# Kernel optimization log

Measured on AMD Instinct MI355X. Metric: run time of the kernel, lower is better.

## Reference

```python
import jax, jax.numpy as jnp
import numpy as np

D = 768        # memory_dim
H = 16         # num_heads
DH = D // H    # head dim (hidden_size)
SCALING = 0.25 # inverse temperature beta
STEPS = 5      # update_steps_max (fixed-count; eps early-exit ignored)
TOP_K = 4
LN_EPS = 1e-5


def setup_inputs() -> dict:
    key = jax.random.key(0)
    ks = jax.random.split(key, 8)
    B, N = 2, 100000
    inp = {
        "query_embedding": jax.random.normal(ks[0], (B, D), jnp.float32),
        "memory": jax.random.normal(ks[1], (N, D), jnp.float32),
        # LayerNorm (affine) params: state pattern (query), stored pattern (keys), pattern projection (values)
        "ln_q_g": jnp.ones((D,), jnp.float32), "ln_q_b": jnp.zeros((D,), jnp.float32),
        "ln_s_g": jnp.ones((D,), jnp.float32), "ln_s_b": jnp.zeros((D,), jnp.float32),
        "ln_p_g": jnp.ones((D,), jnp.float32), "ln_p_b": jnp.zeros((D,), jnp.float32),
        # association-space projections and output projection
        "Wq": 0.02 * jax.random.normal(ks[2], (D, D), jnp.float32), "bq": jnp.zeros((D,), jnp.float32),
        "Wk": 0.02 * jax.random.normal(ks[3], (D, D), jnp.float32), "bk": jnp.zeros((D,), jnp.float32),
        "Wv": 0.02 * jax.random.normal(ks[4], (D, D), jnp.float32), "bv": jnp.zeros((D,), jnp.float32),
        "Wo": 0.02 * jax.random.normal(ks[5], (D, D), jnp.float32), "bo": jnp.zeros((D,), jnp.float32),
    }
    return inp


def _layer_norm(x, g, b):
    m = jnp.mean(x, axis=-1, keepdims=True)
    v = jnp.var(x, axis=-1, keepdims=True)
    return (x - m) * jax.lax.rsqrt(v + LN_EPS) * g + b


def _hopfield_pool(query, memory, ln_q_g, ln_q_b, ln_s_g, ln_s_b, ln_p_g, ln_p_b,
                   Wq, bq, Wk, bk, Wv, bv, Wo, bo):
    B = query.shape[0]
    # projections (memory is shared across the batch, so project once: (N, D))
    q0 = _layer_norm(query, ln_q_g, ln_q_b) @ Wq + bq        # (B, D)
    k = (_layer_norm(memory, ln_s_g, ln_s_b) @ Wk + bk).reshape(-1, H, DH)   # (N, H, DH)
    v = (_layer_norm(memory, ln_p_g, ln_p_b) @ Wv + bv).reshape(-1, H, DH)   # (N, H, DH)

    q = (SCALING * q0).reshape(B, H, DH)                      # (B, H, DH)
    attn = jax.nn.softmax(jnp.einsum("bhd,nhd->bhn", q, k), axis=-1)
    for _ in range(STEPS):  # iterative Hopfield state updates
        q = SCALING * jnp.einsum("bhn,nhd->bhd", attn, k)
        attn = jax.nn.softmax(jnp.einsum("bhd,nhd->bhn", q, k), axis=-1)
    out = jnp.einsum("bhn,nhd->bhd", attn, v).reshape(B, D)   # concat heads
    return out @ Wo + bo                                      # (B, D) pooled


def reference(query_embedding, memory, ln_q_g, ln_q_b, ln_s_g, ln_s_b, ln_p_g, ln_p_b,
              Wq, bq, Wk, bk, Wv, bv, Wo, bo):
    pooled = _hopfield_pool(query_embedding, memory, ln_q_g, ln_q_b, ln_s_g, ln_s_b,
                            ln_p_g, ln_p_b, Wq, bq, Wk, bk, Wv, bv, Wo, bo)
    pooled_norm = pooled / jnp.linalg.norm(pooled, axis=-1, keepdims=True)
    memory_norm = memory / jnp.linalg.norm(memory, axis=-1, keepdims=True)
    similarities = pooled_norm @ memory_norm.T                # (B, N)
    _, top_indices = jax.lax.top_k(similarities, TOP_K)       # (B, TOP_K)
    return top_indices, pooled
```

## Files before the change

kernel.cpp:

```cpp
#include <hip/hip_runtime.h>
#include <cstdio>
#include <cstdint>


#define NMEM 100000
#define NPAD 100096
#define HOPB 1024
#define CBLK 98
#define UKS  512
#define UROWS 196
#define SCALING_ 0.25f

typedef __attribute__((ext_vector_type(8))) short bf16x8;
typedef __attribute__((ext_vector_type(4))) float f32x4;

__device__ __forceinline__ unsigned short f2bf(float f) {
  union { float f; unsigned u; } c; c.f = f;
  unsigned u = c.u + 0x7fffu + ((c.u >> 16) & 1u);
  return (unsigned short)(u >> 16);
}
__device__ __forceinline__ float bf2f(unsigned short h) {
  union { unsigned u; float f; } c; c.u = ((unsigned)h) << 16;
  return c.f;
}
__device__ __forceinline__ void gl_lds16(const void* g, void* l) {
  __builtin_amdgcn_global_load_lds(
      (const __attribute__((address_space(1))) unsigned int*)g,
      (__attribute__((address_space(3))) unsigned int*)l, 16, 0, 0);
}

__device__ __forceinline__ bool bet(float s, int n, float v, int i) {
  return (s > v) || (s == v && n < i);
}
struct Top4 {
  float v0, v1, v2, v3;
  int   i0, i1, i2, i3;
  __device__ __forceinline__ void init() {
    v0 = v1 = v2 = v3 = -INFINITY;
    i0 = i1 = i2 = i3 = 0x7fffffff;
  }
  __device__ __forceinline__ void ins(float s, int n) {
    bool c0 = bet(s, n, v0, i0), c1 = bet(s, n, v1, i1);
    bool c2 = bet(s, n, v2, i2), c3 = bet(s, n, v3, i3);
    float w0 = c0 ? s : v0;             int j0 = c0 ? n : i0;
    float w1 = c0 ? v0 : (c1 ? s : v1); int j1 = c0 ? i0 : (c1 ? n : i1);
    float w2 = c1 ? v1 : (c2 ? s : v2); int j2 = c1 ? i1 : (c2 ? n : i2);
    float w3 = c2 ? v2 : (c3 ? s : v3); int j3 = c2 ? i2 : (c3 ? n : i3);
    v0 = w0; v1 = w1; v2 = w2; v3 = w3;
    i0 = j0; i1 = j1; i2 = j2; i3 = j3;
  }
};
__device__ __forceinline__ void bfly(Top4& a, int omax) {
  for (int o = omax; o >= 1; o >>= 1) {
    float w0 = __shfl_xor(a.v0, o), w1 = __shfl_xor(a.v1, o);
    float w2 = __shfl_xor(a.v2, o), w3 = __shfl_xor(a.v3, o);
    int   j0 = __shfl_xor(a.i0, o), j1 = __shfl_xor(a.i1, o);
    int   j2 = __shfl_xor(a.i2, o), j3 = __shfl_xor(a.i3, o);
    a.ins(w0, j0); a.ins(w1, j1); a.ins(w2, j2); a.ins(w3, j3);
  }
}

__global__ __launch_bounds__(256) void k_fold_wt(const float* __restrict__ Wk,
                                                 const float* __restrict__ Wv,
                                                 const float* __restrict__ gs,
                                                 const float* __restrict__ gp,
                                                 unsigned short* __restrict__ WT) {
  __shared__ float ts[64][65];
  int d0 = blockIdx.x * 64, j0 = blockIdx.y * 64, z = blockIdx.z;
  const float* W = z ? Wv : Wk;
  const float* g = z ? gp : gs;
  int t = threadIdx.x, c = t & 63, r4 = t >> 6;
#pragma unroll
  for (int p = 0; p < 16; ++p) {
    int r = p * 4 + r4;
    ts[r][c] = g[d0 + r] * W[(size_t)(d0 + r) * 768 + j0 + c];
  }
  __syncthreads();
#pragma unroll
  for (int p = 0; p < 16; ++p) {
    int jr = p * 4 + r4;
    WT[(size_t)(z * 768 + j0 + jr) * 768 + d0 + c] = f2bf(ts[c][jr]);
  }
}

__global__ __launch_bounds__(256) void k_fold_bias(const float* __restrict__ Wk,
                                                   const float* __restrict__ Wv,
                                                   const float* __restrict__ bs,
                                                   const float* __restrict__ bp,
                                                   float* __restrict__ PB) {
  int jc = blockIdx.x, dz = blockIdx.y, t = threadIdx.x;
  int j = jc * 256 + t;
  const float* W  = (j < 768) ? Wk : Wv;
  const float* bb = (j < 768) ? bs : bp;
  int jj = (j < 768) ? j : j - 768;
  float a = 0.f;
  int dend = dz * 96 + 96;
  for (int d = dz * 96; d < dend; ++d) a = fmaf(bb[d], W[(size_t)d * 768 + jj], a);
  PB[dz * 1536 + j] = a;
}

__global__ __launch_bounds__(256) void k_bias_red(const float* __restrict__ PB,
                                                  const float* __restrict__ bk,
                                                  const float* __restrict__ bv,
                                                  float* __restrict__ BKV) {
  int j = blockIdx.x * 256 + threadIdx.x;
  float a = (j < 768) ? bk[j] : bv[j - 768];
#pragma unroll
  for (int dz = 0; dz < 8; ++dz) a += PB[dz * 1536 + j];
  BKV[j] = a;
}

__global__ __launch_bounds__(256) void k_q0(const float* __restrict__ qe,
                                            const float* __restrict__ gq,
                                            const float* __restrict__ bq_ln,
                                            const float* __restrict__ Wq,
                                            const float* __restrict__ bq,
                                            float* __restrict__ qbuf) {
  int b = blockIdx.y, jc = blockIdx.x, t = threadIdx.x;
  __shared__ float xs[768];
  __shared__ float sred[16];
  __shared__ float pr[256];
  float x0 = qe[b * 768 + t], x1 = qe[b * 768 + 256 + t], x2 = qe[b * 768 + 512 + t];
  float s = x0 + x1 + x2, s2 = x0 * x0 + x1 * x1 + x2 * x2;
#pragma unroll
  for (int o = 32; o >= 1; o >>= 1) { s += __shfl_xor(s, o); s2 += __shfl_xor(s2, o); }
  int lane = t & 63, w = t >> 6;
  if (lane == 0) { sred[w] = s; sred[8 + w] = s2; }
  __syncthreads();
  s  = sred[0] + sred[1] + sred[2] + sred[3];
  s2 = sred[8] + sred[9] + sred[10] + sred[11];
  float mean = s * (1.f / 768.f);
  float var  = s2 * (1.f / 768.f) - mean * mean;
  float rstd = rsqrtf(var + 1e-5f);
  xs[t]       = (x0 - mean) * rstd * gq[t]       + bq_ln[t];
  xs[t + 256] = (x1 - mean) * rstd * gq[t + 256] + bq_ln[t + 256];
  xs[t + 512] = (x2 - mean) * rstd * gq[t + 512] + bq_ln[t + 512];
  __syncthreads();
  int j = jc * 64 + lane;
  float a = 0.f;
  int d0 = w * 192;
  for (int d = d0; d < d0 + 192; ++d) a = fmaf(xs[d], Wq[(size_t)d * 768 + j], a);
  pr[t] = a;
  __syncthreads();
  if (t < 64) {
    float sv = pr[t] + pr[64 + t] + pr[128 + t] + pr[192 + t];
    int j2 = jc * 64 + t;
    qbuf[b * 768 + j2] = SCALING_ * (sv + bq[j2]);
  }
}

__global__ __launch_bounds__(256) void k_ln(const float* __restrict__ mem,
                                            unsigned short* __restrict__ XH,
                                            float* __restrict__ rnorm) {
  int gw = (blockIdx.x * 256 + threadIdx.x) >> 6;
  int lane = threadIdx.x & 63;
  int n0 = gw * 25;
  int nend = n0 + 25; if (nend > NPAD) nend = NPAD;
  for (int n = n0; n < nend; ++n) {
    ushort4* orow = (ushort4*)(XH + (size_t)n * 768);
    if (n >= NMEM) {
      ushort4 z; z.x = z.y = z.z = z.w = 0;
      orow[lane] = z; orow[lane + 64] = z; orow[lane + 128] = z;
      continue;
    }
    const float4* r = (const float4*)(mem + (size_t)n * 768);
    float4 x0 = r[lane], x1 = r[lane + 64], x2 = r[lane + 128];
    float s  = x0.x + x0.y + x0.z + x0.w + x1.x + x1.y + x1.z + x1.w +
               x2.x + x2.y + x2.z + x2.w;
    float s2 = x0.x * x0.x + x0.y * x0.y + x0.z * x0.z + x0.w * x0.w +
               x1.x * x1.x + x1.y * x1.y + x1.z * x1.z + x1.w * x1.w +
               x2.x * x2.x + x2.y * x2.y + x2.z * x2.z + x2.w * x2.w;
#pragma unroll
    for (int o = 32; o >= 1; o >>= 1) { s += __shfl_xor(s, o); s2 += __shfl_xor(s2, o); }
    float mean = s * (1.f / 768.f);
    float var  = s2 * (1.f / 768.f) - mean * mean;
    float rstd = rsqrtf(var + 1e-5f);
    if (lane == 0) rnorm[n] = rsqrtf(s2);
    ushort4 o0, o1, o2;
    o0.x = f2bf((x0.x - mean) * rstd); o0.y = f2bf((x0.y - mean) * rstd);
    o0.z = f2bf((x0.z - mean) * rstd); o0.w = f2bf((x0.w - mean) * rstd);
    o1.x = f2bf((x1.x - mean) * rstd); o1.y = f2bf((x1.y - mean) * rstd);
    o1.z = f2bf((x1.z - mean) * rstd); o1.w = f2bf((x1.w - mean) * rstd);
    o2.x = f2bf((x2.x - mean) * rstd); o2.y = f2bf((x2.y - mean) * rstd);
    o2.z = f2bf((x2.z - mean) * rstd); o2.w = f2bf((x2.w - mean) * rstd);
    orow[lane] = o0; orow[lane + 64] = o1; orow[lane + 128] = o2;
  }
}

__global__ __launch_bounds__(256) void k_gemm(const unsigned short* __restrict__ XH,
                                              const unsigned short* __restrict__ WT,
                                              const float* __restrict__ BKV,
                                              unsigned short* __restrict__ KB) {
  __shared__ __align__(16) unsigned short SM[32768];
  int f = blockIdx.x;
  int xcd = f & 7, s = f >> 3;
  int g = s / 6, jt = s - g * 6;
  int mt = g * 8 + xcd;
  if (mt >= 782) return;
  int m0 = mt * 128, j0 = jt * 128;
  int tid = threadIdx.x;
  int wave = tid >> 6, lane = tid & 63;
  int wm = wave >> 1, wn = wave & 1;
  int fr_r = lane & 15, chb = lane >> 4;
  f32x4 acc[4][4] = {};

  auto stage = [&](int kt, int bb) {
    unsigned short* As = SM + bb * 16384;
    unsigned short* Bs = As + 8192;
    int k0 = kt * 64;
#pragma unroll
    for (int it = 0; it < 4; ++it) {
      int c = it * 256 + tid;
      int row = c >> 3, kk = c & 7;
      int src = (kk ^ (row & 7)) * 8;
      gl_lds16(XH + (size_t)(m0 + row) * 768 + k0 + src, As + c * 8);
      gl_lds16(WT + (size_t)(j0 + row) * 768 + k0 + src, Bs + c * 8);
    }
  };

  stage(0, 0);
  int cur = 0;
  for (int kt = 0; kt < 12; ++kt) {
    if (kt < 11) {
      stage(kt + 1, cur ^ 1);
      asm volatile("s_waitcnt vmcnt(8)" ::: "memory");
    } else {
      asm volatile("s_waitcnt vmcnt(0)" ::: "memory");
    }
    __builtin_amdgcn_s_barrier();
    __builtin_amdgcn_sched_barrier(0);
    const unsigned short* As = SM + cur * 16384;
    const unsigned short* Bs = As + 8192;
    __builtin_amdgcn_s_setprio(1);
#pragma unroll
    for (int ks = 0; ks < 2; ++ks) {
      bf16x8 af[4], bfr[4];
#pragma unroll
      for (int ff = 0; ff < 4; ++ff) {
        int ra = wm * 64 + ff * 16 + fr_r;
        int rb = wn * 64 + ff * 16 + fr_r;
        int cha  = ((ks * 4 + chb) ^ (ra & 7)) * 8;
        int chbb = ((ks * 4 + chb) ^ (rb & 7)) * 8;
        af[ff]  = *(const bf16x8*)(As + ra * 64 + cha);
        bfr[ff] = *(const bf16x8*)(Bs + rb * 64 + chbb);
      }
#pragma unroll
      for (int fm = 0; fm < 4; ++fm)
#pragma unroll
        for (int fn = 0; fn < 4; ++fn)
          acc[fm][fn] = __builtin_amdgcn_mfma_f32_16x16x32_bf16(af[fm], bfr[fn],
                                                                acc[fm][fn], 0, 0, 0);
    }
    __builtin_amdgcn_s_setprio(0);
    __builtin_amdgcn_s_barrier();
    __builtin_amdgcn_sched_barrier(0);
    cur ^= 1;
  }
  int cr = (lane >> 4) * 4, cc = lane & 15;
#pragma unroll
  for (int fm = 0; fm < 4; ++fm)
#pragma unroll
    for (int fn = 0; fn < 4; ++fn) {
      int col = wn * 64 + fn * 16 + cc;
      float bias = BKV[j0 + col];
      int rb = (wm * 64 + fm * 16 + cr) * 128 + col;
#pragma unroll
      for (int i = 0; i < 4; ++i)
        SM[rb + i * 128] = f2bf(acc[fm][fn][i] + bias);
    }
  __syncthreads();
#pragma unroll
  for (int it = 0; it < 8; ++it) {
    int c = it * 256 + tid;
    int row = c >> 4, cg = c & 15;
    *(bf16x8*)(KB + (size_t)(m0 + row) * 768 + j0 + cg * 8) =
        *(const bf16x8*)(SM + row * 128 + cg * 8);
  }
}

__device__ __forceinline__ void load6(const unsigned short* p, float* o) {
  ushort2 a = *(const ushort2*)(p);
  ushort2 b = *(const ushort2*)(p + 2);
  ushort2 c = *(const ushort2*)(p + 4);
  o[0] = bf2f(a.x); o[1] = bf2f(a.y);
  o[2] = bf2f(b.x); o[3] = bf2f(b.y);
  o[4] = bf2f(c.x); o[5] = bf2f(c.y);
}

__global__ __launch_bounds__(256) void k_hop(const unsigned short* __restrict__ KB,
                                             const float* __restrict__ qin,
                                             float* __restrict__ pa,
                                             float* __restrict__ pl) {
  __shared__ float red[4][768];
  __shared__ float redl[4][128];
  int tid = threadIdx.x, blk = blockIdx.x;
  int w = tid >> 6, lane = tid & 63;
  int hb = w & 1, sub = w >> 1;
  float qv0[6], qv1[6];
  const float* qb = qin + hb * 384 + lane * 6;
#pragma unroll
  for (int j = 0; j < 6; ++j) { qv0[j] = qb[j]; qv1[j] = qb[768 + j]; }
  float l0 = 0.f, l1 = 0.f;
  float acc0[6] = {}, acc1[6] = {};
  int n0 = blk * CBLK + sub * 49;
  int nend = n0 + 49;
  if (nend > NMEM) nend = NMEM;
#pragma unroll 4
  for (int n = n0; n < nend; ++n) {
    const unsigned short* ks = KB + (size_t)n * 768 + hb * 384 + lane * 6;
    float kf[6]; load6(ks, kf);
    float sc0 = 0.f, sc1 = 0.f;
#pragma unroll
    for (int j = 0; j < 6; ++j) {
      sc0 = fmaf(kf[j], qv0[j], sc0);
      sc1 = fmaf(kf[j], qv1[j], sc1);
    }
#pragma unroll
    for (int o = 1; o < 8; o <<= 1) {
      sc0 += __shfl_xor(sc0, o);
      sc1 += __shfl_xor(sc1, o);
    }
    float e0 = __expf(sc0);
    float e1 = __expf(sc1);
    l0 += e0; l1 += e1;
#pragma unroll
    for (int j = 0; j < 6; ++j) {
      acc0[j] = fmaf(e0, kf[j], acc0[j]);
      acc1[j] = fmaf(e1, kf[j], acc1[j]);
    }
  }
#pragma unroll
  for (int j = 0; j < 6; ++j) {
    red[w][lane * 12 + j]     = acc0[j];
    red[w][lane * 12 + 6 + j] = acc1[j];
  }
  redl[w][lane * 2]     = l0;
  redl[w][lane * 2 + 1] = l1;
  __syncthreads();
  if (sub == 0) {
#pragma unroll
    for (int j = 0; j < 6; ++j) {
      acc0[j] += red[w + 2][lane * 12 + j];
      acc1[j] += red[w + 2][lane * 12 + 6 + j];
    }
    l0 += redl[w + 2][lane * 2];
    l1 += redl[w + 2][lane * 2 + 1];
    int h = hb * 8 + (lane >> 3), p = lane & 7;
    size_t b0 = ((size_t)(h * 2 + 0) * HOPB + blk) * 48 + p * 6;
    size_t b1 = ((size_t)(h * 2 + 1) * HOPB + blk) * 48 + p * 6;
#pragma unroll
    for (int j = 0; j < 6; ++j) { pa[b0 + j] = acc0[j]; pa[b1 + j] = acc1[j]; }
    if (p == 0) {
      pl[(size_t)(h * 2 + 0) * HOPB + blk] = l0;
      pl[(size_t)(h * 2 + 1) * HOPB + blk] = l1;
    }
  }
}

__global__ __launch_bounds__(256) void k_hred(const float* __restrict__ pa,
                                              const float* __restrict__ pl,
                                              float* __restrict__ qout) {
  int b = blockIdx.x & 1, h = blockIdx.x >> 1;
  __shared__ float sred[4];
  __shared__ float p3[256];
  int t = threadIdx.x, lane = t & 63, w = t >> 6;
  size_t mlb = (size_t)(h * 2 + b) * HOPB;
  float ll = 0.f;
  for (int i = t; i < HOPB; i += 256) ll += pl[mlb + i];
#pragma unroll
  for (int o = 32; o >= 1; o >>= 1) ll += __shfl_xor(ll, o);
  if (lane == 0) sred[w] = ll;
  __syncthreads();
  float ltot = sred[0] + sred[1] + sred[2] + sred[3];
  int d = t & 63, seg = t >> 6;
  float a = 0.f;
  if (d < 48) {
#pragma unroll 4
    for (int i = seg; i < HOPB; i += 4)
      a += pa[(mlb + i) * 48 + d];
  }
  p3[seg * 64 + d] = a;
  __syncthreads();
  if (t < 48) {
    float av = p3[t] + p3[64 + t] + p3[128 + t] + p3[192 + t];
    qout[b * 768 + h * 48 + t] = SCALING_ * (av / ltot);
  }
}

__global__ __launch_bounds__(256) void k_escore(const unsigned short* __restrict__ KB,
                                                const float* __restrict__ qin,
                                                float* __restrict__ S,
                                                float* __restrict__ pl) {
  __shared__ float redl[4][128];
  int tid = threadIdx.x, blk = blockIdx.x;
  int w = tid >> 6, lane = tid & 63;
  int hb = w & 1, sub = w >> 1;
  float qv0[6], qv1[6];
  const float* qb = qin + hb * 384 + lane * 6;
#pragma unroll
  for (int j = 0; j < 6; ++j) { qv0[j] = qb[j]; qv1[j] = qb[768 + j]; }
  float l0 = 0.f, l1 = 0.f;
  int hl = lane >> 3, p = lane & 7;
  int h = hb * 8 + hl;
  int n0 = blk * CBLK + sub * 49;
  int nend = n0 + 49;
  if (nend > NMEM) nend = NMEM;
#pragma unroll 4
  for (int n = n0; n < nend; ++n) {
    const unsigned short* ks = KB + (size_t)n * 768 + hb * 384 + lane * 6;
    float kf[6]; load6(ks, kf);
    float sc0 = 0.f, sc1 = 0.f;
#pragma unroll
    for (int j = 0; j < 6; ++j) {
      sc0 = fmaf(kf[j], qv0[j], sc0);
      sc1 = fmaf(kf[j], qv1[j], sc1);
    }
#pragma unroll
    for (int o = 1; o < 8; o <<= 1) {
      sc0 += __shfl_xor(sc0, o);
      sc1 += __shfl_xor(sc1, o);
    }
    if (p == 0) {
      S[(size_t)n * 32 + h]      = sc0;
      S[(size_t)n * 32 + 16 + h] = sc1;
    }
    l0 += __expf(sc0);
    l1 += __expf(sc1);
  }
  redl[w][lane * 2]     = l0;
  redl[w][lane * 2 + 1] = l1;
  __syncthreads();
  if (sub == 0) {
    l0 += redl[w + 2][lane * 2];
    l1 += redl[w + 2][lane * 2 + 1];
    if (p == 0) {
      pl[(size_t)(h * 2 + 0) * HOPB + blk] = l0;
      pl[(size_t)(h * 2 + 1) * HOPB + blk] = l1;
    }
  }
}

__global__ __launch_bounds__(256) void k_hredM(const float* __restrict__ pl,
                                               float* __restrict__ C) {
  int b = blockIdx.x & 1, h = blockIdx.x >> 1;
  __shared__ float sred[4];
  int t = threadIdx.x, lane = t & 63, w = t >> 6;
  size_t mlb = (size_t)(h * 2 + b) * HOPB;
  float ll = 0.f;
  for (int i = t; i < HOPB; i += 256) ll += pl[mlb + i];
#pragma unroll
  for (int o = 32; o >= 1; o >>= 1) ll += __shfl_xor(ll, o);
  if (lane == 0) sred[w] = ll;
  __syncthreads();
  if (t == 0) C[b * 16 + h] = logf(sred[0] + sred[1] + sred[2] + sred[3]);
}

__global__ __launch_bounds__(256) void k_upass(const unsigned short* __restrict__ XH,
                                               const float* __restrict__ S,
                                               const float* __restrict__ C,
                                               float* __restrict__ UP) {
  __shared__ float SW[64 * 32];
  __shared__ float cc[32];
  int kb = blockIdx.x, t = threadIdx.x;
  if (t < 32) cc[t] = C[t];
  float a0[32], a1[32], a2[32];
#pragma unroll
  for (int i = 0; i < 32; ++i) { a0[i] = 0.f; a1[i] = 0.f; a2[i] = 0.f; }
  int n0 = kb * UROWS;
  int nend = n0 + UROWS; if (nend > NMEM) nend = NMEM;
  for (int ns = n0; ns < nend; ns += 64) {
    int sub = nend - ns; if (sub > 64) sub = 64;
    __syncthreads();
    for (int i = t; i < sub * 32; i += 256)
      SW[i] = __expf(S[(size_t)ns * 32 + i] - cc[i & 31]);
    __syncthreads();
    for (int r = 0; r < sub; ++r) {
      const unsigned short* xr = XH + (size_t)(ns + r) * 768;
      float x0 = bf2f(xr[t]), x1 = bf2f(xr[t + 256]), x2 = bf2f(xr[t + 512]);
      const float4* w4 = (const float4*)(SW + r * 32);
#pragma unroll
      for (int c = 0; c < 8; ++c) {
        float4 wv = w4[c];
        a0[c * 4 + 0] = fmaf(wv.x, x0, a0[c * 4 + 0]);
        a0[c * 4 + 1] = fmaf(wv.y, x0, a0[c * 4 + 1]);
        a0[c * 4 + 2] = fmaf(wv.z, x0, a0[c * 4 + 2]);
        a0[c * 4 + 3] = fmaf(wv.w, x0, a0[c * 4 + 3]);
        a1[c * 4 + 0] = fmaf(wv.x, x1, a1[c * 4 + 0]);
        a1[c * 4 + 1] = fmaf(wv.y, x1, a1[c * 4 + 1]);
        a1[c * 4 + 2] = fmaf(wv.z, x1, a1[c * 4 + 2]);
        a1[c * 4 + 3] = fmaf(wv.w, x1, a1[c * 4 + 3]);
        a2[c * 4 + 0] = fmaf(wv.x, x2, a2[c * 4 + 0]);
        a2[c * 4 + 1] = fmaf(wv.y, x2, a2[c * 4 + 1]);
        a2[c * 4 + 2] = fmaf(wv.z, x2, a2[c * 4 + 2]);
        a2[c * 4 + 3] = fmaf(wv.w, x2, a2[c * 4 + 3]);
      }
    }
  }
#pragma unroll
  for (int bh = 0; bh < 32; ++bh) {
    size_t base = ((size_t)kb * 32 + bh) * 768;
    UP[base + t]       = a0[bh];
    UP[base + 256 + t] = a1[bh];
    UP[base + 512 + t] = a2[bh];
  }
}

__global__ __launch_bounds__(256) void k_ured(const float* __restrict__ UP,
                                              float* __restrict__ U) {
  int o = blockIdx.x * 256 + threadIdx.x;
  float s0 = 0.f, s1 = 0.f, s2 = 0.f, s3 = 0.f;
#pragma unroll 4
  for (int kb = 0; kb < UKS; kb += 4) {
    s0 += UP[(size_t)(kb + 0) * 24576 + o];
    s1 += UP[(size_t)(kb + 1) * 24576 + o];
    s2 += UP[(size_t)(kb + 2) * 24576 + o];
    s3 += UP[(size_t)(kb + 3) * 24576 + o];
  }
  U[o] = (s0 + s1) + (s2 + s3);
}

__global__ __launch_bounds__(256) void k_outproj(const float* __restrict__ U,
                                                 const unsigned short* __restrict__ WT,
                                                 const float* __restrict__ BKV,
                                                 float* __restrict__ outa) {
  int gw = blockIdx.x * 4 + (threadIdx.x >> 6);
  int lane = threadIdx.x & 63;
  int b = gw >= 768;
  int j = gw - b * 768;
  int h = j / 48;
  const float* u = U + (size_t)(b * 16 + h) * 768;
  const unsigned short* wr = WT + (size_t)(768 + j) * 768;
  float a = 0.f;
  for (int d = lane; d < 768; d += 64) a = fmaf(u[d], bf2f(wr[d]), a);
#pragma unroll
  for (int o = 32; o >= 1; o >>= 1) a += __shfl_xor(a, o);
  if (lane == 0) outa[b * 768 + j] = a + BKV[768 + j];
}

__global__ __launch_bounds__(256) void k_pooled(const float* __restrict__ outa,
                                                const float* __restrict__ Wo,
                                                const float* __restrict__ bo,
                                                float* __restrict__ dp) {
  __shared__ float xs[768];
  __shared__ float pr[256];
  int b = blockIdx.y, jc = blockIdx.x, t = threadIdx.x;
  xs[t]       = outa[b * 768 + t];
  xs[t + 256] = outa[b * 768 + 256 + t];
  xs[t + 512] = outa[b * 768 + 512 + t];
  __syncthreads();
  int w = t >> 6, lane = t & 63;
  int j = jc * 64 + lane;
  float a = 0.f;
  int d0 = w * 192;
  for (int d = d0; d < d0 + 192; ++d) a = fmaf(xs[d], Wo[(size_t)d * 768 + j], a);
  pr[t] = a;
  __syncthreads();
  if (t < 64) {
    float sv = pr[t] + pr[64 + t] + pr[128 + t] + pr[192 + t];
    int j2 = jc * 64 + t;
    dp[b * 768 + j2] = sv + bo[j2];
  }
}

__global__ __launch_bounds__(256) void k_pnorm(const float* __restrict__ dp,
                                               float* __restrict__ PN) {
  int b = blockIdx.x, t = threadIdx.x;
  __shared__ float sred[8];
  float x0 = dp[b * 768 + t], x1 = dp[b * 768 + 256 + t], x2 = dp[b * 768 + 512 + t];
  float s2 = x0 * x0 + x1 * x1 + x2 * x2;
#pragma unroll
  for (int o = 32; o >= 1; o >>= 1) s2 += __shfl_xor(s2, o);
  int lane = t & 63, w = t >> 6;
  if (lane == 0) sred[w] = s2;
  __syncthreads();
  float tot = sred[0] + sred[1] + sred[2] + sred[3];
  float rs = rsqrtf(tot);
  PN[b * 768 + t]       = x0 * rs;
  PN[b * 768 + 256 + t] = x1 * rs;
  PN[b * 768 + 512 + t] = x2 * rs;
}

__global__ __launch_bounds__(256) void k_sim(const float* __restrict__ mem,
                                             const float* __restrict__ PN,
                                             const float* __restrict__ rnorm,
                                             float* __restrict__ tval,
                                             int* __restrict__ tidx) {
  int gw = (blockIdx.x * 256 + threadIdx.x) >> 6;
  int lane = threadIdx.x & 63;
  const float4* pa = (const float4*)(PN);
  const float4* pb = (const float4*)(PN + 768);
  float4 qa0 = pa[lane], qa1 = pa[lane + 64], qa2 = pa[lane + 128];
  float4 qb0 = pb[lane], qb1 = pb[lane + 64], qb2 = pb[lane + 128];
  Top4 t0, t1; t0.init(); t1.init();
  int n0 = gw * 13;
  int nend = n0 + 13; if (nend > NMEM) nend = NMEM;
  for (int n = n0; n < nend; ++n) {
    const float4* r = (const float4*)(mem + (size_t)n * 768);
    float4 x0 = r[lane], x1 = r[lane + 64], x2 = r[lane + 128];
    float d0 = x0.x * qa0.x + x0.y * qa0.y + x0.z * qa0.z + x0.w * qa0.w +
               x1.x * qa1.x + x1.y * qa1.y + x1.z * qa1.z + x1.w * qa1.w +
               x2.x * qa2.x + x2.y * qa2.y + x2.z * qa2.z + x2.w * qa2.w;
    float d1 = x0.x * qb0.x + x0.y * qb0.y + x0.z * qb0.z + x0.w * qb0.w +
               x1.x * qb1.x + x1.y * qb1.y + x1.z * qb1.z + x1.w * qb1.w +
               x2.x * qb2.x + x2.y * qb2.y + x2.z * qb2.z + x2.w * qb2.w;
#pragma unroll
    for (int o = 32; o >= 1; o >>= 1) { d0 += __shfl_xor(d0, o); d1 += __shfl_xor(d1, o); }
    float rn = rnorm[n];
    t0.ins(d0 * rn, n);
    t1.ins(d1 * rn, n);
  }
  if (lane == 0) {
    int base = gw * 8;
    tval[base + 0] = t0.v0; tval[base + 1] = t0.v1; tval[base + 2] = t0.v2; tval[base + 3] = t0.v3;
    tval[base + 4] = t1.v0; tval[base + 5] = t1.v1; tval[base + 6] = t1.v2; tval[base + 7] = t1.v3;
    tidx[base + 0] = t0.i0; tidx[base + 1] = t0.i1; tidx[base + 2] = t0.i2; tidx[base + 3] = t0.i3;
    tidx[base + 4] = t1.i0; tidx[base + 5] = t1.i1; tidx[base + 6] = t1.i2; tidx[base + 7] = t1.i3;
  }
}

__global__ __launch_bounds__(256) void k_top1(const float* __restrict__ tval,
                                              const int* __restrict__ tidx,
                                              float* __restrict__ ptv,
                                              int* __restrict__ pti) {
  __shared__ float lv[4][8];
  __shared__ int   li[4][8];
  int z = blockIdx.x, t = threadIdx.x;
  int lane = t & 63, w = t >> 6;
  int wv = z * 256 + t;
  Top4 a, b; a.init(); b.init();
#pragma unroll
  for (int r = 0; r < 4; ++r) {
    a.ins(tval[wv * 8 + r],     tidx[wv * 8 + r]);
    b.ins(tval[wv * 8 + 4 + r], tidx[wv * 8 + 4 + r]);
  }
  bfly(a, 32);
  bfly(b, 32);
  if (lane == 0) {
    lv[w][0] = a.v0; lv[w][1] = a.v1; lv[w][2] = a.v2; lv[w][3] = a.v3;
    lv[w][4] = b.v0; lv[w][5] = b.v1; lv[w][6] = b.v2; lv[w][7] = b.v3;
    li[w][0] = a.i0; li[w][1] = a.i1; li[w][2] = a.i2; li[w][3] = a.i3;
    li[w][4] = b.i0; li[w][5] = b.i1; li[w][6] = b.i2; li[w][7] = b.i3;
  }
  __syncthreads();
  if (t < 2) {
    Top4 m_; m_.init();
#pragma unroll
    for (int w2 = 0; w2 < 4; ++w2)
#pragma unroll
      for (int r = 0; r < 4; ++r) m_.ins(lv[w2][t * 4 + r], li[w2][t * 4 + r]);
    int base = z * 8 + t * 4;
    ptv[base + 0] = m_.v0; ptv[base + 1] = m_.v1;
    ptv[base + 2] = m_.v2; ptv[base + 3] = m_.v3;
    pti[base + 0] = m_.i0; pti[base + 1] = m_.i1;
    pti[base + 2] = m_.i2; pti[base + 3] = m_.i3;
  }
}

__global__ __launch_bounds__(64) void k_top2(const float* __restrict__ ptv,
                                             const int* __restrict__ pti,
                                             float* __restrict__ dout) {
  int t = threadIdx.x;
  int half = t >> 5, e = t & 31;
  Top4 a; a.init();
#pragma unroll
  for (int r = 0; r < 4; ++r)
    a.ins(ptv[e * 8 + half * 4 + r], pti[e * 8 + half * 4 + r]);
  bfly(a, 16);
  if (e == 0) {
    dout[half * 4 + 0] = (float)a.i0;
    dout[half * 4 + 1] = (float)a.i1;
    dout[half * 4 + 2] = (float)a.i2;
    dout[half * 4 + 3] = (float)a.i3;
  }
}

extern "C" void kernel_launch(void* const* d_in, const int* in_sizes, int n_in,
                              void* d_out, int out_size, void* d_ws, size_t ws_size,
                              hipStream_t stream) {
  const float* qe     = (const float*)d_in[0];
  const float* mem    = (const float*)d_in[1];
  const float* ln_q_g = (const float*)d_in[2];
  const float* ln_q_b = (const float*)d_in[3];
  const float* ln_s_g = (const float*)d_in[4];
  const float* ln_s_b = (const float*)d_in[5];
  const float* ln_p_g = (const float*)d_in[6];
  const float* ln_p_b = (const float*)d_in[7];
  const float* Wq = (const float*)d_in[8];  const float* bq = (const float*)d_in[9];
  const float* Wk = (const float*)d_in[10]; const float* bk = (const float*)d_in[11];
  const float* Wv = (const float*)d_in[12]; const float* bv = (const float*)d_in[13];
  const float* Wo = (const float*)d_in[14]; const float* bo = (const float*)d_in[15];

  char* w = (char*)d_ws;
  size_t off = 0;
  auto alloc = [&](size_t bytes) {
    size_t o = off;
    off += (bytes + 255) & ~(size_t)255;
    return o;
  };
  unsigned short* WT   = (unsigned short*)(w + alloc((size_t)1536 * 768 * 2));
  float*          PB   = (float*)(w + alloc(8 * 1536 * 4));
  float*          BKV  = (float*)(w + alloc(1536 * 4));
  float*          QBUF = (float*)(w + alloc(1536 * 4));
  float*          OUTA = (float*)(w + alloc(1536 * 4));
  float*          PN   = (float*)(w + alloc(1536 * 4));
  float*          CML  = (float*)(w + alloc(32 * 4));
  float*          UBUF = (float*)(w + alloc((size_t)24576 * 4));
  float*          RNORM= (float*)(w + alloc((size_t)NPAD * 4));
  unsigned short* XH   = (unsigned short*)(w + alloc((size_t)NPAD * 768 * 2));
  unsigned short* KB   = (unsigned short*)(w + alloc((size_t)NPAD * 768 * 2));
  float*          PA   = (float*)(w + alloc((size_t)32 * HOPB * 48 * 4));
  float*          PL   = (float*)(w + alloc((size_t)32 * HOPB * 4));
  float*          SB   = (float*)(w + alloc((size_t)NMEM * 32 * 4));
  float*          UP   = (float*)(w + alloc((size_t)UKS * 24576 * 4));
  float*          TVAL = (float*)(w + alloc((size_t)8192 * 8 * 4));
  int*            TIDX = (int*)(w + alloc((size_t)8192 * 8 * 4));
  float*          PTV  = (float*)(w + alloc((size_t)32 * 8 * 4));
  int*            PTI  = (int*)(w + alloc((size_t)32 * 8 * 4));
  if (off > ws_size) {
    fprintf(stderr, "[hopfield] ws too small: need %zu have %zu\n", off, ws_size);
    return;
  }
  float* dout = (float*)d_out;

  k_fold_wt  <<<dim3(12, 12, 2), 256, 0, stream>>>(Wk, Wv, ln_s_g, ln_p_g, WT);
  k_fold_bias<<<dim3(6, 8), 256, 0, stream>>>(Wk, Wv, ln_s_b, ln_p_b, PB);
  k_bias_red <<<6, 256, 0, stream>>>(PB, bk, bv, BKV);
  k_q0       <<<dim3(12, 2), 256, 0, stream>>>(qe, ln_q_g, ln_q_b, Wq, bq, QBUF);
  k_ln       <<<1024, 256, 0, stream>>>(mem, XH, RNORM);
  k_gemm     <<<98 * 6 * 8, 256, 0, stream>>>(XH, WT, BKV, KB);
  for (int step = 0; step < 5; ++step) {
    k_hop    <<<HOPB, 256, 0, stream>>>(KB, QBUF, PA, PL);
    k_hred   <<<32, 256, 0, stream>>>(PA, PL, QBUF);
  }
  k_escore   <<<HOPB, 256, 0, stream>>>(KB, QBUF, SB, PL);
  k_hredM    <<<32, 256, 0, stream>>>(PL, CML);
  k_upass    <<<UKS, 256, 0, stream>>>(XH, SB, CML, UP);
  k_ured     <<<96, 256, 0, stream>>>(UP, UBUF);
  k_outproj  <<<384, 256, 0, stream>>>(UBUF, WT, BKV, OUTA);
  k_pooled   <<<dim3(12, 2), 256, 0, stream>>>(OUTA, Wo, bo, dout + 8);
  k_pnorm    <<<2, 256, 0, stream>>>(dout + 8, PN);
  k_sim      <<<2048, 256, 0, stream>>>(mem, PN, RNORM, TVAL, TIDX);
  k_top1     <<<32, 256, 0, stream>>>(TVAL, TIDX, PTV, PTI);
  k_top2     <<<1, 64, 0, stream>>>(PTV, PTI, dout);
}
```

Measured before the change: 851.1 us.

## Replace per-step reduction kernels with atomic accumulation into rotating buffers

Removes the separate k_hred and k_hredM reduction kernels. Each k_hop and k_escore block now atomically adds its partial accumulators and softmax denominators into small per-step buffers. The next step folds the normalization (scaling/L) into its query load, and block 0 zeroes the buffer two steps ahead. This cuts six kernel launches and the large partial-sum round trips through memory, at the cost of global atomic contention and a nondeterministic summation order.

```diff
diff --git a/kernel.cpp b/kernel.cpp
--- a/kernel.cpp
+++ b/kernel.cpp
@@ -115,11 +115,16 @@
                                             const float* __restrict__ bq_ln,
                                             const float* __restrict__ Wq,
                                             const float* __restrict__ bq,
-                                            float* __restrict__ qbuf) {
+                                            float* __restrict__ ACCb,
+                                            float* __restrict__ Lb) {
   int b = blockIdx.y, jc = blockIdx.x, t = threadIdx.x;
   __shared__ float xs[768];
   __shared__ float sred[16];
   __shared__ float pr[256];
+  if (jc == 0 && b == 0) {
+    for (int i = t; i < 1536; i += 256) ACCb[1536 + i] = 0.f;
+    if (t < 32) { Lb[t] = 1.0f; Lb[32 + t] = 0.f; }
+  }
   float x0 = qe[b * 768 + t], x1 = qe[b * 768 + 256 + t], x2 = qe[b * 768 + 512 + t];
   float s = x0 + x1 + x2, s2 = x0 * x0 + x1 * x1 + x2 * x2;
 #pragma unroll
@@ -145,7 +150,8 @@
   if (t < 64) {
     float sv = pr[t] + pr[64 + t] + pr[128 + t] + pr[192 + t];
     int j2 = jc * 64 + t;
-    qbuf[b * 768 + j2] = SCALING_ * (sv + bq[j2]);
+    int h = j2 / 48, dh = j2 - h * 48;
+    ACCb[(h * 2 + b) * 48 + dh] = sv + bq[j2];
   }
 }
 
@@ -288,18 +294,31 @@
 }
 
 __global__ __launch_bounds__(256) void k_hop(const unsigned short* __restrict__ KB,
-                                             const float* __restrict__ qin,
-                                             float* __restrict__ pa,
-                                             float* __restrict__ pl) {
+                                             float* __restrict__ ACCb,
+                                             float* __restrict__ Lb,
+                                             int s) {
   __shared__ float red[4][768];
   __shared__ float redl[4][128];
   int tid = threadIdx.x, blk = blockIdx.x;
   int w = tid >> 6, lane = tid & 63;
   int hb = w & 1, sub = w >> 1;
+  const float* Ap  = ACCb + s * 1536;
+  const float* Lp  = Lb + s * 32;
+  float* An  = ACCb + (s + 1) * 1536;
+  float* Ln_ = Lb + (s + 1) * 32;
+  if (blk == 0) {
+    for (int i = tid; i < 1536; i += 256) ACCb[(s + 2) * 1536 + i] = 0.f;
+    if (tid < 32) Lb[(s + 2) * 32 + tid] = 0.f;
+  }
+  int h = hb * 8 + (lane >> 3), p = lane & 7;
+  float rl0 = SCALING_ / Lp[h * 2 + 0];
+  float rl1 = SCALING_ / Lp[h * 2 + 1];
   float qv0[6], qv1[6];
-  const float* qb = qin + hb * 384 + lane * 6;
-#pragma unroll
-  for (int j = 0; j < 6; ++j) { qv0[j] = qb[j]; qv1[j] = qb[768 + j]; }
+#pragma unroll
+  for (int j = 0; j < 6; ++j) {
+    qv0[j] = rl0 * Ap[(h * 2 + 0) * 48 + p * 6 + j];
+    qv1[j] = rl1 * Ap[(h * 2 + 1) * 48 + p * 6 + j];
+  }
   float l0 = 0.f, l1 = 0.f;
   float acc0[6] = {}, acc1[6] = {};
   int n0 = blk * CBLK + sub * 49;
@@ -345,63 +364,37 @@
     }
     l0 += redl[w + 2][lane * 2];
     l1 += redl[w + 2][lane * 2 + 1];
-    int h = hb * 8 + (lane >> 3), p = lane & 7;
-    size_t b0 = ((size_t)(h * 2 + 0) * HOPB + blk) * 48 + p * 6;
-    size_t b1 = ((size_t)(h * 2 + 1) * HOPB + blk) * 48 + p * 6;
-#pragma unroll
-    for (int j = 0; j < 6; ++j) { pa[b0 + j] = acc0[j]; pa[b1 + j] = acc1[j]; }
+#pragma unroll
+    for (int j = 0; j < 6; ++j) {
+      atomicAdd(&An[(h * 2 + 0) * 48 + p * 6 + j], acc0[j]);
+      atomicAdd(&An[(h * 2 + 1) * 48 + p * 6 + j], acc1[j]);
+    }
     if (p == 0) {
-      pl[(size_t)(h * 2 + 0) * HOPB + blk] = l0;
-      pl[(size_t)(h * 2 + 1) * HOPB + blk] = l1;
-    }
-  }
-}
-
-__global__ __launch_bounds__(256) void k_hred(const float* __restrict__ pa,
-                                              const float* __restrict__ pl,
-                                              float* __restrict__ qout) {
-  int b = blockIdx.x & 1, h = blockIdx.x >> 1;
-  __shared__ float sred[4];
-  __shared__ float p3[256];
-  int t = threadIdx.x, lane = t & 63, w = t >> 6;
-  size_t mlb = (size_t)(h * 2 + b) * HOPB;
-  float ll = 0.f;
-  for (int i = t; i < HOPB; i += 256) ll += pl[mlb + i];
-#pragma unroll
-  for (int o = 32; o >= 1; o >>= 1) ll += __shfl_xor(ll, o);
-  if (lane == 0) sred[w] = ll;
-  __syncthreads();
-  float ltot = sred[0] + sred[1] + sred[2] + sred[3];
-  int d = t & 63, seg = t >> 6;
-  float a = 0.f;
-  if (d < 48) {
-#pragma unroll 4
-    for (int i = seg; i < HOPB; i += 4)
-      a += pa[(mlb + i) * 48 + d];
-  }
-  p3[seg * 64 + d] = a;
-  __syncthreads();
-  if (t < 48) {
-    float av = p3[t] + p3[64 + t] + p3[128 + t] + p3[192 + t];
-    qout[b * 768 + h * 48 + t] = SCALING_ * (av / ltot);
+      atomicAdd(&Ln_[h * 2 + 0], l0);
+      atomicAdd(&Ln_[h * 2 + 1], l1);
+    }
   }
 }
 
 __global__ __launch_bounds__(256) void k_escore(const unsigned short* __restrict__ KB,
-                                                const float* __restrict__ qin,
+                                                const float* __restrict__ Ap,
+                                                const float* __restrict__ Lp,
                                                 float* __restrict__ S,
-                                                float* __restrict__ pl) {
+                                                float* __restrict__ LF) {
   __shared__ float redl[4][128];
   int tid = threadIdx.x, blk = blockIdx.x;
   int w = tid >> 6, lane = tid & 63;
   int hb = w & 1, sub = w >> 1;
+  int h = hb * 8 + (lane >> 3), p = lane & 7;
+  float rl0 = SCALING_ / Lp[h * 2 + 0];
+  float rl1 = SCALING_ / Lp[h * 2 + 1];
   float qv0[6], qv1[6];
-  const float* qb = qin + hb * 384 + lane * 6;
-#pragma unroll
-  for (int j = 0; j < 6; ++j) { qv0[j] = qb[j]; qv1[j] = qb[768 + j]; }
+#pragma unroll
+  for (int j = 0; j < 6; ++j) {
+    qv0[j] = rl0 * Ap[(h * 2 + 0) * 48 + p * 6 + j];
+    qv1[j] = rl1 * Ap[(h * 2 + 1) * 48 + p * 6 + j];
+  }
   float l0 = 0.f, l1 = 0.f;
-  int hl = lane >> 3, p = lane & 7;
-  int h = hb * 8 + hl;
   int n0 = blk * CBLK + sub * 49;
   int nend = n0 + 49;
   if (nend > NMEM) nend = NMEM;
@@ -434,35 +427,20 @@
     l0 += redl[w + 2][lane * 2];
     l1 += redl[w + 2][lane * 2 + 1];
     if (p == 0) {
-      pl[(size_t)(h * 2 + 0) * HOPB + blk] = l0;
-      pl[(size_t)(h * 2 + 1) * HOPB + blk] = l1;
-    }
-  }
-}
-
-__global__ __launch_bounds__(256) void k_hredM(const float* __restrict__ pl,
-                                               float* __restrict__ C) {
-  int b = blockIdx.x & 1, h = blockIdx.x >> 1;
-  __shared__ float sred[4];
-  int t = threadIdx.x, lane = t & 63, w = t >> 6;
-  size_t mlb = (size_t)(h * 2 + b) * HOPB;
-  float ll = 0.f;
-  for (int i = t; i < HOPB; i += 256) ll += pl[mlb + i];
-#pragma unroll
-  for (int o = 32; o >= 1; o >>= 1) ll += __shfl_xor(ll, o);
-  if (lane == 0) sred[w] = ll;
-  __syncthreads();
-  if (t == 0) C[b * 16 + h] = logf(sred[0] + sred[1] + sred[2] + sred[3]);
+      atomicAdd(&LF[h * 2 + 0], l0);
+      atomicAdd(&LF[h * 2 + 1], l1);
+    }
+  }
 }
 
 __global__ __launch_bounds__(256) void k_upass(const unsigned short* __restrict__ XH,
                                                const float* __restrict__ S,
-                                               const float* __restrict__ C,
+                                               const float* __restrict__ LF,
                                                float* __restrict__ UP) {
   __shared__ float SW[64 * 32];
   __shared__ float cc[32];
   int kb = blockIdx.x, t = threadIdx.x;
-  if (t < 32) cc[t] = C[t];
+  if (t < 32) cc[t] = 1.0f / LF[t];
   float a0[32], a1[32], a2[32];
 #pragma unroll
   for (int i = 0; i < 32; ++i) { a0[i] = 0.f; a1[i] = 0.f; a2[i] = 0.f; }
@@ -472,7 +450,7 @@
     int sub = nend - ns; if (sub > 64) sub = 64;
     __syncthreads();
     for (int i = t; i < sub * 32; i += 256)
-      SW[i] = __expf(S[(size_t)ns * 32 + i] - cc[i & 31]);
+      SW[i] = __expf(S[(size_t)ns * 32 + i]) * cc[i & 31];
     __syncthreads();
     for (int r = 0; r < sub; ++r) {
       const unsigned short* xr = XH + (size_t)(ns + r) * 768;
@@ -700,16 +678,14 @@
   unsigned short* WT   = (unsigned short*)(w + alloc((size_t)1536 * 768 * 2));
   float*          PB   = (float*)(w + alloc(8 * 1536 * 4));
   float*          BKV  = (float*)(w + alloc(1536 * 4));
-  float*          QBUF = (float*)(w + alloc(1536 * 4));
+  float*          ACCB = (float*)(w + alloc(7 * 1536 * 4));
+  float*          LB   = (float*)(w + alloc(7 * 32 * 4));
   float*          OUTA = (float*)(w + alloc(1536 * 4));
   float*          PN   = (float*)(w + alloc(1536 * 4));
-  float*          CML  = (float*)(w + alloc(32 * 4));
   float*          UBUF = (float*)(w + alloc((size_t)24576 * 4));
   float*          RNORM= (float*)(w + alloc((size_t)NPAD * 4));
   unsigned short* XH   = (unsigned short*)(w + alloc((size_t)NPAD * 768 * 2));
   unsigned short* KB   = (unsigned short*)(w + alloc((size_t)NPAD * 768 * 2));
-  float*          PA   = (float*)(w + alloc((size_t)32 * HOPB * 48 * 4));
-  float*          PL   = (float*)(w + alloc((size_t)32 * HOPB * 4));
   float*          SB   = (float*)(w + alloc((size_t)NMEM * 32 * 4));
   float*          UP   = (float*)(w + alloc((size_t)UKS * 24576 * 4));
   float*          TVAL = (float*)(w + alloc((size_t)8192 * 8 * 4));
@@ -725,16 +701,14 @@
   k_fold_wt  <<<dim3(12, 12, 2), 256, 0, stream>>>(Wk, Wv, ln_s_g, ln_p_g, WT);
   k_fold_bias<<<dim3(6, 8), 256, 0, stream>>>(Wk, Wv, ln_s_b, ln_p_b, PB);
   k_bias_red <<<6, 256, 0, stream>>>(PB, bk, bv, BKV);
-  k_q0       <<<dim3(12, 2), 256, 0, stream>>>(qe, ln_q_g, ln_q_b, Wq, bq, QBUF);
+  k_q0       <<<dim3(12, 2), 256, 0, stream>>>(qe, ln_q_g, ln_q_b, Wq, bq, ACCB, LB);
   k_ln       <<<1024, 256, 0, stream>>>(mem, XH, RNORM);
   k_gemm     <<<98 * 6 * 8, 256, 0, stream>>>(XH, WT, BKV, KB);
-  for (int step = 0; step < 5; ++step) {
-    k_hop    <<<HOPB, 256, 0, stream>>>(KB, QBUF, PA, PL);
-    k_hred   <<<32, 256, 0, stream>>>(PA, PL, QBUF);
-  }
-  k_escore   <<<HOPB, 256, 0, stream>>>(KB, QBUF, SB, PL);
-  k_hredM    <<<32, 256, 0, stream>>>(PL, CML);
-  k_upass    <<<UKS, 256, 0, stream>>>(XH, SB, CML, UP);
+  for (int s = 0; s < 5; ++s)
+    k_hop    <<<HOPB, 256, 0, stream>>>(KB, ACCB, LB, s);
+  k_escore   <<<HOPB, 256, 0, stream>>>(KB, ACCB + 5 * 1536, LB + 5 * 32, SB,
+                                        LB + 6 * 32);
+  k_upass    <<<UKS, 256, 0, stream>>>(XH, SB, LB + 6 * 32, UP);
   k_ured     <<<96, 256, 0, stream>>>(UP, UBUF);
   k_outproj  <<<384, 256, 0, stream>>>(UBUF, WT, BKV, OUTA);
   k_pooled   <<<dim3(12, 2), 256, 0, stream>>>(OUTA, Wo, bo, dout + 8);
```

Result: slower. 1.508 ms (+77.2%).
